# Optimization experiments

Measured on AMD Instinct MI355X. Metric: run time of the kernel, lower is better.

Reference implementation:

```python
import jax, jax.numpy as jnp
import numpy as np

B, H, W = 8, 64, 64
DIM, NH, WS = 768, 12, 14
HD = DIM // NH            # head dim = 64
N = WS * WS               # tokens per window = 196
PAD = (WS - H % WS) % WS  # 6 -> padded grid 70
HP, WP = H + PAD, W + PAD
NW = (HP // WS) * (WP // WS)  # 25 windows
EPS = 1e-5


def _layer_norm(x, w, b):
    mu = x.mean(-1, keepdims=True)
    var = ((x - mu) ** 2).mean(-1, keepdims=True)
    return (x - mu) * jax.lax.rsqrt(var + EPS) * w + b


def _window_partition(x):
    # [B,H,W,C] -> [B*NW, WS, WS, C] with zero padding
    x = jnp.pad(x, ((0, 0), (0, PAD), (0, PAD), (0, 0)))
    x = x.reshape(B, HP // WS, WS, WP // WS, WS, DIM)
    return x.transpose(0, 1, 3, 2, 4, 5).reshape(-1, WS, WS, DIM)


def _window_unpartition(w):
    x = w.reshape(B, HP // WS, WP // WS, WS, WS, DIM)
    x = x.transpose(0, 1, 3, 2, 4, 5).reshape(B, HP, WP, DIM)
    return x[:, :H, :W, :]


def _rel_table(rel_pos):
    # get_rel_pos with q_size==k_size==WS, rel_pos already (2*WS-1, HD):
    # Rh[i,j] = rel_pos[i - j + WS - 1]; summed over channel dim (batched_index_and_sum sums last dim)
    coords = jnp.arange(WS)[:, None] - jnp.arange(WS)[None, :] + (WS - 1)
    return rel_pos[coords].sum(-1)  # (WS, WS)


def _attention(w, q_idx, k_idx, qkv_w, qkv_b, proj_w, proj_b, rel_h, rel_w):
    Bp = w.shape[0]  # B*NW
    xq = w.reshape(Bp, N, DIM)
    qkv = xq @ qkv_w + qkv_b                                  # (Bp, N, 3*DIM)
    qkv = qkv.reshape(Bp, N, 3, NH, HD).transpose(2, 0, 3, 1, 4)
    qkv = qkv.reshape(3, Bp * NH, N, HD)
    q, k, v = qkv[0], qkv[1], qkv[2]
    scale = HD ** -0.5
    attn = jnp.einsum('bqc,bkc->bqk', q * scale, k)           # (Bp*NH, N, N)
    # decomposed rel-pos bias via irregular per-batch index gather
    Sh, Sw = _rel_table(rel_h), _rel_table(rel_w)
    qr, qc = q_idx // WS, q_idx % WS                          # (Bp*NH, N)
    kr, kc = k_idx // WS, k_idx % WS
    bias = Sh[qr[:, :, None], kr[:, None, :]] + Sw[qc[:, :, None], kc[:, None, :]]
    attn = jax.nn.softmax(attn + bias, axis=-1)
    out = jnp.einsum('bqk,bkc->bqc', attn, v)                 # (Bp*NH, N, HD)
    out = out.reshape(Bp, NH, N, HD).transpose(0, 2, 1, 3).reshape(Bp, WS, WS, DIM)
    return out @ proj_w + proj_b


def _block(x, q_idx, k_idx, ln1_w, ln1_b, ln2_w, ln2_b, qkv_w, qkv_b,
           proj_w, proj_b, rel_h, rel_w, mlp_w1, mlp_b1, mlp_w2, mlp_b2):
    shortcut = x
    h = _layer_norm(x, ln1_w, ln1_b)
    win = _window_partition(h)
    win = _attention(win, q_idx, k_idx, qkv_w, qkv_b, proj_w, proj_b, rel_h, rel_w)
    h = _window_unpartition(win)
    x = shortcut + h
    m = _layer_norm(x, ln2_w, ln2_b)
    m = jax.nn.gelu(m @ mlp_w1 + mlp_b1, approximate=False) @ mlp_w2 + mlp_b2
    return x + m


def setup_inputs() -> dict:
    key = jax.random.key(0)
    ks = jax.random.split(key, 12)
    f = lambda k, s: jax.random.normal(k, s, jnp.float32) * 0.02
    return {
        'x': jax.random.normal(ks[0], (B, H, W, DIM), jnp.float32),
        'q_idx': jnp.sort(jax.random.randint(ks[1], (B * NW * NH, N), 0, N), axis=-1),
        'k_idx': jnp.sort(jax.random.randint(ks[2], (B * NW * NH, N), 0, N), axis=-1),
        'ln1_w': jnp.ones((DIM,), jnp.float32), 'ln1_b': jnp.zeros((DIM,), jnp.float32),
        'ln2_w': jnp.ones((DIM,), jnp.float32), 'ln2_b': jnp.zeros((DIM,), jnp.float32),
        'qkv_w': f(ks[3], (DIM, 3 * DIM)), 'qkv_b': jnp.zeros((3 * DIM,), jnp.float32),
        'proj_w': f(ks[4], (DIM, DIM)), 'proj_b': jnp.zeros((DIM,), jnp.float32),
        'rel_h': f(ks[5], (2 * WS - 1, HD)), 'rel_w': f(ks[6], (2 * WS - 1, HD)),
        'mlp_w1': f(ks[7], (DIM, 4 * DIM)), 'mlp_b1': jnp.zeros((4 * DIM,), jnp.float32),
        'mlp_w2': f(ks[8], (4 * DIM, DIM)), 'mlp_b2': jnp.zeros((DIM,), jnp.float32),
    }


def reference(x, q_idx, k_idx, ln1_w, ln1_b, ln2_w, ln2_b, qkv_w, qkv_b,
              proj_w, proj_b, rel_h, rel_w, mlp_w1, mlp_b1, mlp_w2, mlp_b2):
    return _block(x, q_idx, k_idx, ln1_w, ln1_b, ln2_w, ln2_b, qkv_w, qkv_b,
                  proj_w, proj_b, rel_h, rel_w, mlp_w1, mlp_b1, mlp_w2, mlp_b2)
```

## Files before the change

kernel.cpp:

```cpp
#include <hip/hip_runtime.h>


typedef __bf16 bf16x8 __attribute__((ext_vector_type(8)));
typedef float f32x4 __attribute__((ext_vector_type(4)));
typedef unsigned int u32x4 __attribute__((ext_vector_type(4)));

__device__ __forceinline__ unsigned short f2bf(float f) {
  unsigned int u = __builtin_bit_cast(unsigned int, f);
  u += 0x7FFFu + ((u >> 16) & 1u);
  return (unsigned short)(u >> 16);
}

__device__ __forceinline__ bf16x8 ld8(const unsigned short* p) {
  return __builtin_bit_cast(bf16x8, *(const u32x4*)p);
}

__global__ void transpose_w(const float* __restrict__ in,
                            unsigned short* __restrict__ out, int K, int N) {
  __shared__ float t[32][33];
  int n = blockIdx.x * 32 + threadIdx.x;
  int kb = blockIdx.y * 32;
#pragma unroll
  for (int i = 0; i < 4; i++) {
    int k = kb + threadIdx.y + i * 8;
    t[threadIdx.y + i * 8][threadIdx.x] = in[(size_t)k * N + n];
  }
  __syncthreads();
  int k2 = kb + threadIdx.x;
#pragma unroll
  for (int i = 0; i < 4; i++) {
    int n2 = blockIdx.x * 32 + threadIdx.y + i * 8;
    out[(size_t)n2 * K + k2] = f2bf(t[threadIdx.x][threadIdx.y + i * 8]);
  }
}

__global__ void shsw_kernel(const float* __restrict__ rh,
                            const float* __restrict__ rw,
                            float* __restrict__ o) {
  int t = threadIdx.x;
  if (t < 196) {
    int i = t / 14, j = t % 14, d = i - j + 13;
    float sh = 0.f, sw = 0.f;
    for (int c = 0; c < 64; c++) {
      sh += rh[d * 64 + c];
      sw += rw[d * 64 + c];
    }
    o[t] = sh;
    o[196 + t] = sw;
  }
}

__global__ __launch_bounds__(256) void ln_kernel(
    const float* __restrict__ xin, const float* __restrict__ w,
    const float* __restrict__ b, unsigned short* __restrict__ out,
    int windowed) {
  __shared__ float red[8];
  __shared__ float ms[2];
  const int tid = threadIdx.x;
  const int blk = blockIdx.x;
  const float* xr = xin + (size_t)blk * 768;
  float v0 = xr[tid], v1 = xr[tid + 256], v2 = xr[tid + 512];
  float s = v0 + v1 + v2;
  float q = v0 * v0 + v1 * v1 + v2 * v2;
#pragma unroll
  for (int off = 32; off > 0; off >>= 1) {
    s += __shfl_down(s, off, 64);
    q += __shfl_down(q, off, 64);
  }
  const int wv = tid >> 6, lane = tid & 63;
  if (lane == 0) { red[wv] = s; red[4 + wv] = q; }
  __syncthreads();
  if (tid == 0) {
    float st = red[0] + red[1] + red[2] + red[3];
    float qt = red[4] + red[5] + red[6] + red[7];
    float mu = st * (1.0f / 768.0f);
    float var = qt * (1.0f / 768.0f) - mu * mu;
    ms[0] = mu;
    ms[1] = rsqrtf(var + 1e-5f);
  }
  __syncthreads();
  float mu = ms[0], sc = ms[1];
  unsigned short* dst;
  if (windowed) {
    int bb = blk >> 12, rem = blk & 4095, h = rem >> 6, ww = rem & 63;
    int win = (bb * 5 + h / 14) * 5 + ww / 14;
    int t = (h % 14) * 14 + (ww % 14);
    dst = out + ((size_t)win * 196 + t) * 768;
  } else {
    dst = out + (size_t)blk * 768;
  }
  dst[tid] = f2bf((v0 - mu) * sc * w[tid] + b[tid]);
  dst[tid + 256] = f2bf((v1 - mu) * sc * w[tid + 256] + b[tid + 256]);
  dst[tid + 512] = f2bf((v2 - mu) * sc * w[tid + 512] + b[tid + 512]);
}

template <int EPI>
__global__ __launch_bounds__(256, 2) void gemm_bt(
    const unsigned short* __restrict__ A, const unsigned short* __restrict__ Bt,
    const float* __restrict__ bias, int M, int N, int K,
    unsigned short* __restrict__ obf, float* __restrict__ of,
    const float* __restrict__ resid) {
  __shared__ __align__(16) unsigned short As[128 * 40];
  __shared__ __align__(16) unsigned short Bs[128 * 40];
  const int tid = threadIdx.x;
  const int lane = tid & 63, wv = tid >> 6;
  const int ln15 = lane & 15, quad = lane >> 4;
  const int wm = wv & 1, wn = wv >> 1;
  const int m0 = blockIdx.y * 128, n0 = blockIdx.x * 128;

  const int ra0 = tid >> 2, ka0 = (tid & 3) * 8;
  const int ra1 = ra0 + 64;
  const unsigned short* pA0 = A + (size_t)min(m0 + ra0, M - 1) * K + ka0;
  const unsigned short* pA1 = A + (size_t)min(m0 + ra1, M - 1) * K + ka0;
  const unsigned short* pB0 = Bt + (size_t)(n0 + ra0) * K + ka0;
  const unsigned short* pB1 = Bt + (size_t)(n0 + ra1) * K + ka0;

  const f32x4 fz = {0.f, 0.f, 0.f, 0.f};
  f32x4 acc[4][4];
#pragma unroll
  for (int i = 0; i < 4; i++)
#pragma unroll
    for (int j = 0; j < 4; j++) acc[i][j] = fz;

  u32x4 va0 = *(const u32x4*)(pA0);
  u32x4 va1 = *(const u32x4*)(pA1);
  u32x4 vb0 = *(const u32x4*)(pB0);
  u32x4 vb1 = *(const u32x4*)(pB1);

  for (int kt = 0; kt < K; kt += 32) {
    __syncthreads();
    *(u32x4*)(As + ra0 * 40 + ka0) = va0;
    *(u32x4*)(As + ra1 * 40 + ka0) = va1;
    *(u32x4*)(Bs + ra0 * 40 + ka0) = vb0;
    *(u32x4*)(Bs + ra1 * 40 + ka0) = vb1;
    __syncthreads();
    if (kt + 32 < K) {
      va0 = *(const u32x4*)(pA0 + kt + 32);
      va1 = *(const u32x4*)(pA1 + kt + 32);
      vb0 = *(const u32x4*)(pB0 + kt + 32);
      vb1 = *(const u32x4*)(pB1 + kt + 32);
    }
    bf16x8 af[4], bv[4];
#pragma unroll
    for (int t = 0; t < 4; t++) {
      af[t] = ld8(As + (wm * 64 + t * 16 + ln15) * 40 + quad * 8);
      bv[t] = ld8(Bs + (wn * 64 + t * 16 + ln15) * 40 + quad * 8);
    }
#pragma unroll
    for (int i = 0; i < 4; i++)
#pragma unroll
      for (int j = 0; j < 4; j++)
        acc[i][j] =
            __builtin_amdgcn_mfma_f32_16x16x32_bf16(af[i], bv[j], acc[i][j], 0, 0, 0);
  }

#pragma unroll
  for (int i = 0; i < 4; i++) {
#pragma unroll
    for (int j = 0; j < 4; j++) {
      const int col = n0 + wn * 64 + j * 16 + ln15;
      const float bc = bias[col];
#pragma unroll
      for (int g = 0; g < 4; g++) {
        const int row = m0 + wm * 64 + i * 16 + quad * 4 + g;
        if (row >= M) continue;
        float v = acc[i][j][g] + bc;
        if constexpr (EPI == 0) {
          obf[(size_t)row * N + col] = f2bf(v);
        } else if constexpr (EPI == 2) {
          float gl = 0.5f * v * (1.0f + erff(v * 0.70710678118f));
          obf[(size_t)row * N + col] = f2bf(gl);
        } else if constexpr (EPI == 1) {
          int win = row / 196, t = row - win * 196;
          int b = win / 25, wg = win - b * 25;
          int wr = wg / 5, wc = wg - wr * 5;
          int h = wr * 14 + t / 14;
          int w = wc * 14 + (t % 14);
          if (h < 64 && w < 64) {
            size_t oi = (((size_t)(b * 64 + h)) * 64 + w) * 768 + col;
            of[oi] = v + resid[oi];
          }
        } else {
          size_t oi = (size_t)row * N + col;
          of[oi] += v;
        }
      }
    }
  }
}

__global__ __launch_bounds__(256, 2) void attn_kernel(
    const unsigned short* __restrict__ qkv, const int* __restrict__ q_idx,
    const int* __restrict__ k_idx, const float* __restrict__ shsw,
    unsigned short* __restrict__ attnout) {
  __shared__ __align__(16) unsigned short Vt[64][232];
  __shared__ __align__(16) unsigned short Pst[4][16 * 232];
  __shared__ float Shs[196], Sws[196];
  __shared__ short qr14a[208], qc14a[208], kra[208], kca[208];

  const int tid = threadIdx.x;
  const int blk = blockIdx.x;
  const int win = blk / 12, head = blk % 12;
  const int lane = tid & 63, wv = tid >> 6;
  const int ln15 = lane & 15, quad = lane >> 4;
  const unsigned short* qg = qkv + (size_t)win * 196 * 2304;

  {
    unsigned int* vz = (unsigned int*)&Vt[0][0];
    for (int i = tid; i < 64 * 232 / 2; i += 256) vz[i] = 0u;
    unsigned int* pz = (unsigned int*)&Pst[0][0];
    for (int i = tid; i < 4 * 16 * 232 / 2; i += 256) pz[i] = 0u;
  }
  for (int i = tid; i < 196 * 64; i += 256) {
    int r = i >> 6, c = i & 63;
    Vt[c][r] = qg[(size_t)r * 2304 + 1536 + head * 64 + c];
  }
  for (int i = tid; i < 208; i += 256) {
    if (i < 196) {
      Shs[i] = shsw[i];
      Sws[i] = shsw[196 + i];
    }
    int q = (i < 196) ? q_idx[(size_t)blk * 196 + i] : 0;
    int k = (i < 196) ? k_idx[(size_t)blk * 196 + i] : 0;
    qr14a[i] = (short)((q / 14) * 14);
    qc14a[i] = (short)((q % 14) * 14);
    kra[i] = (short)(k / 14);
    kca[i] = (short)(k % 14);
  }
  __syncthreads();

  const f32x4 fz = {0.f, 0.f, 0.f, 0.f};
  unsigned short* strip = &Pst[wv][0];

  for (int mt = wv; mt < 13; mt += 4) {
    int qrow = mt * 16 + ln15;
    int qrc = (qrow < 196) ? qrow : 0;
    const unsigned short* qrp = qg + (size_t)qrc * 2304 + head * 64 + quad * 8;
    bf16x8 aq0 = ld8(qrp);
    bf16x8 aq1 = ld8(qrp + 32);

    f32x4 sacc[13];
#pragma unroll
    for (int nt = 0; nt < 13; nt++) {
      sacc[nt] = fz;
      int krow = nt * 16 + ln15;
      if (krow > 195) krow = 0;
      const unsigned short* krp =
          qg + (size_t)krow * 2304 + 768 + head * 64 + quad * 8;
      bf16x8 bk0 = ld8(krp);
      bf16x8 bk1 = ld8(krp + 32);
      sacc[nt] = __builtin_amdgcn_mfma_f32_16x16x32_bf16(aq0, bk0, sacc[nt], 0, 0, 0);
      sacc[nt] = __builtin_amdgcn_mfma_f32_16x16x32_bf16(aq1, bk1, sacc[nt], 0, 0, 0);
    }

    const int r0 = mt * 16 + quad * 4;
    int qi[4], qci[4];
#pragma unroll
    for (int g = 0; g < 4; g++) {
      qi[g] = qr14a[r0 + g];
      qci[g] = qc14a[r0 + g];
    }
    float rmax[4] = {-1e30f, -1e30f, -1e30f, -1e30f};
#pragma unroll
    for (int nt = 0; nt < 13; nt++) {
      int col = nt * 16 + ln15;
      int kr_ = kra[col], kc_ = kca[col];
#pragma unroll
      for (int g = 0; g < 4; g++) {
        float v = sacc[nt][g] * 0.125f + Shs[qi[g] + kr_] + Sws[qci[g] + kc_];
        if (col >= 196) v = -1e30f;
        sacc[nt][g] = v;
        rmax[g] = fmaxf(rmax[g], v);
      }
    }
#pragma unroll
    for (int off = 1; off < 16; off <<= 1)
#pragma unroll
      for (int g = 0; g < 4; g++)
        rmax[g] = fmaxf(rmax[g], __shfl_xor(rmax[g], off, 16));
    float rsum[4] = {0.f, 0.f, 0.f, 0.f};
#pragma unroll
    for (int nt = 0; nt < 13; nt++) {
      int col = nt * 16 + ln15;
#pragma unroll
      for (int g = 0; g < 4; g++) {
        float p = (col >= 196) ? 0.f : __expf(sacc[nt][g] - rmax[g]);
        sacc[nt][g] = p;
        rsum[g] += p;
      }
    }
#pragma unroll
    for (int off = 1; off < 16; off <<= 1)
#pragma unroll
      for (int g = 0; g < 4; g++) rsum[g] += __shfl_xor(rsum[g], off, 16);
    float rinv[4];
#pragma unroll
    for (int g = 0; g < 4; g++) rinv[g] = 1.0f / rsum[g];

#pragma unroll
    for (int nt = 0; nt < 13; nt++) {
      int col = nt * 16 + ln15;
#pragma unroll
      for (int g = 0; g < 4; g++)
        strip[(quad * 4 + g) * 232 + col] = f2bf(sacc[nt][g] * rinv[g]);
    }

    f32x4 oacc[4];
#pragma unroll
    for (int c4 = 0; c4 < 4; c4++) oacc[c4] = fz;
#pragma unroll
    for (int ks = 0; ks < 7; ks++) {
      bf16x8 ap = ld8(strip + ln15 * 232 + ks * 32 + quad * 8);
#pragma unroll
      for (int c4 = 0; c4 < 4; c4++) {
        bf16x8 bvv = ld8(&Vt[c4 * 16 + ln15][ks * 32 + quad * 8]);
        oacc[c4] = __builtin_amdgcn_mfma_f32_16x16x32_bf16(ap, bvv, oacc[c4], 0, 0, 0);
      }
    }
#pragma unroll
    for (int c4 = 0; c4 < 4; c4++)
#pragma unroll
      for (int g = 0; g < 4; g++) {
        int row = r0 + g;
        if (row < 196)
          attnout[((size_t)win * 196 + row) * 768 + head * 64 + c4 * 16 + ln15] =
              f2bf(oacc[c4][g]);
      }
  }
}

extern "C" void kernel_launch(void* const* d_in, const int* in_sizes, int n_in,
                              void* d_out, int out_size, void* d_ws,
                              size_t ws_size, hipStream_t stream) {
  const float* x = (const float*)d_in[0];
  const int* q_idx = (const int*)d_in[1];
  const int* k_idx = (const int*)d_in[2];
  const float* ln1w = (const float*)d_in[3];
  const float* ln1b = (const float*)d_in[4];
  const float* ln2w = (const float*)d_in[5];
  const float* ln2b = (const float*)d_in[6];
  const float* qkvw = (const float*)d_in[7];
  const float* qkvb = (const float*)d_in[8];
  const float* projw = (const float*)d_in[9];
  const float* projb = (const float*)d_in[10];
  const float* relh = (const float*)d_in[11];
  const float* relw = (const float*)d_in[12];
  const float* w1 = (const float*)d_in[13];
  const float* b1 = (const float*)d_in[14];
  const float* w2 = (const float*)d_in[15];
  const float* b2 = (const float*)d_in[16];
  float* out = (float*)d_out;

  char* ws = (char*)d_ws;
  unsigned short* xw = (unsigned short*)ws;
  const size_t offA = 60211200;
  unsigned short* qkv = (unsigned short*)(ws + offA);
  const size_t offB = offA + 201326592;
  unsigned short* qkvwt = (unsigned short*)(ws + offB);
  unsigned short* projwt = qkvwt + 2304 * 768;
  unsigned short* w1t = projwt + 768 * 768;
  unsigned short* w2t = w1t + 3072 * 768;
  float* shsw = (float*)(w2t + 768 * 3072);

  unsigned short* attnout = xw;
  unsigned short* ln2buf = xw;
  unsigned short* mlp1 = qkv;

  hipMemsetAsync(xw, 0, (size_t)39200 * 768 * 2, stream);

  dim3 tb(32, 8);
  transpose_w<<<dim3(2304 / 32, 768 / 32), tb, 0, stream>>>(qkvw, qkvwt, 768, 2304);
  transpose_w<<<dim3(768 / 32, 768 / 32), tb, 0, stream>>>(projw, projwt, 768, 768);
  transpose_w<<<dim3(3072 / 32, 768 / 32), tb, 0, stream>>>(w1, w1t, 768, 3072);
  transpose_w<<<dim3(768 / 32, 3072 / 32), tb, 0, stream>>>(w2, w2t, 3072, 768);
  shsw_kernel<<<1, 256, 0, stream>>>(relh, relw, shsw);

  ln_kernel<<<32768, 256, 0, stream>>>(x, ln1w, ln1b, xw, 1);

  gemm_bt<0><<<dim3(18, 307), 256, 0, stream>>>(xw, qkvwt, qkvb, 39200, 2304,
                                                768, qkv, nullptr, nullptr);
  attn_kernel<<<2400, 256, 0, stream>>>(qkv, q_idx, k_idx, shsw, attnout);

  gemm_bt<1><<<dim3(6, 307), 256, 0, stream>>>(attnout, projwt, projb, 39200,
                                               768, 768, nullptr, out, x);
  ln_kernel<<<32768, 256, 0, stream>>>(out, ln2w, ln2b, ln2buf, 0);

  gemm_bt<2><<<dim3(24, 256), 256, 0, stream>>>(ln2buf, w1t, b1, 32768, 3072,
                                                768, mlp1, nullptr, nullptr);
  gemm_bt<3><<<dim3(6, 256), 256, 0, stream>>>(mlp1, w2t, b2, 32768, 768, 3072,
                                               nullptr, out, nullptr);
  (void)in_sizes; (void)n_in; (void)out_size; (void)ws_size;
}
```

Before: 1.289 ms.

## Load GEMM tiles directly into LDS and remap blocks across XCDs

The GEMM main loop now uses global_load_lds (direct global-to-LDS DMA) instead of register-staged loads, and drops the row padding of 40 in favour of a dense 32-element row stride. It also remaps block IDs so that consecutive tiles land on the same XCD, to improve L2 locality. The register prefetch of the next K tile is removed, so global load latency is no longer overlapped with compute within a block. The unpadded LDS layout may cause bank conflicts on the MFMA fragment reads. There is also no explicit vmcnt wait before the barrier that follows the async LDS writes, which risks reading stale tile data.

Result: no change. 1.267 ms (-1.7%).

```diff
diff --git a/kernel.cpp b/kernel.cpp
--- a/kernel.cpp
+++ b/kernel.cpp
@@ -13,6 +13,13 @@
 
 __device__ __forceinline__ bf16x8 ld8(const unsigned short* p) {
   return __builtin_bit_cast(bf16x8, *(const u32x4*)p);
+}
+
+__device__ __forceinline__ void gload_lds16(const unsigned short* g,
+                                            unsigned short* l) {
+  __builtin_amdgcn_global_load_lds(
+      (const __attribute__((address_space(1))) unsigned int*)g,
+      (__attribute__((address_space(3))) unsigned int*)l, 16, 0, 0);
 }
 
 __global__ void transpose_w(const float* __restrict__ in,
@@ -100,20 +107,31 @@
     const float* __restrict__ bias, int M, int N, int K,
     unsigned short* __restrict__ obf, float* __restrict__ of,
     const float* __restrict__ resid) {
-  __shared__ __align__(16) unsigned short As[128 * 40];
-  __shared__ __align__(16) unsigned short Bs[128 * 40];
+  __shared__ __align__(16) unsigned short As[128 * 32];
+  __shared__ __align__(16) unsigned short Bs[128 * 32];
   const int tid = threadIdx.x;
   const int lane = tid & 63, wv = tid >> 6;
   const int ln15 = lane & 15, quad = lane >> 4;
   const int wm = wv & 1, wn = wv >> 1;
-  const int m0 = blockIdx.y * 128, n0 = blockIdx.x * 128;
+
+  int bid = blockIdx.y * gridDim.x + blockIdx.x;
+  {
+    const int nwg = gridDim.x * gridDim.y;
+    const int q = nwg >> 3, r = nwg & 7;
+    const int xcd = bid & 7, lo = bid >> 3;
+    bid = (xcd < r ? xcd * (q + 1) : r * (q + 1) + (xcd - r) * q) + lo;
+  }
+  const int m0 = (bid / gridDim.x) * 128, n0 = (bid % gridDim.x) * 128;
 
   const int ra0 = tid >> 2, ka0 = (tid & 3) * 8;
-  const int ra1 = ra0 + 64;
   const unsigned short* pA0 = A + (size_t)min(m0 + ra0, M - 1) * K + ka0;
-  const unsigned short* pA1 = A + (size_t)min(m0 + ra1, M - 1) * K + ka0;
+  const unsigned short* pA1 = A + (size_t)min(m0 + ra0 + 64, M - 1) * K + ka0;
   const unsigned short* pB0 = Bt + (size_t)(n0 + ra0) * K + ka0;
-  const unsigned short* pB1 = Bt + (size_t)(n0 + ra1) * K + ka0;
+  const unsigned short* pB1 = Bt + (size_t)(n0 + ra0 + 64) * K + ka0;
+  unsigned short* lA0 = As + tid * 8;
+  unsigned short* lA1 = As + 2048 + tid * 8;
+  unsigned short* lB0 = Bs + tid * 8;
+  unsigned short* lB1 = Bs + 2048 + tid * 8;
 
   const f32x4 fz = {0.f, 0.f, 0.f, 0.f};
   f32x4 acc[4][4];
@@ -122,29 +140,18 @@
 #pragma unroll
     for (int j = 0; j < 4; j++) acc[i][j] = fz;
 
-  u32x4 va0 = *(const u32x4*)(pA0);
-  u32x4 va1 = *(const u32x4*)(pA1);
-  u32x4 vb0 = *(const u32x4*)(pB0);
-  u32x4 vb1 = *(const u32x4*)(pB1);
-
   for (int kt = 0; kt < K; kt += 32) {
     __syncthreads();
-    *(u32x4*)(As + ra0 * 40 + ka0) = va0;
-    *(u32x4*)(As + ra1 * 40 + ka0) = va1;
-    *(u32x4*)(Bs + ra0 * 40 + ka0) = vb0;
-    *(u32x4*)(Bs + ra1 * 40 + ka0) = vb1;
+    gload_lds16(pA0 + kt, lA0);
+    gload_lds16(pA1 + kt, lA1);
+    gload_lds16(pB0 + kt, lB0);
+    gload_lds16(pB1 + kt, lB1);
     __syncthreads();
-    if (kt + 32 < K) {
-      va0 = *(const u32x4*)(pA0 + kt + 32);
-      va1 = *(const u32x4*)(pA1 + kt + 32);
-      vb0 = *(const u32x4*)(pB0 + kt + 32);
-      vb1 = *(const u32x4*)(pB1 + kt + 32);
-    }
     bf16x8 af[4], bv[4];
 #pragma unroll
     for (int t = 0; t < 4; t++) {
-      af[t] = ld8(As + (wm * 64 + t * 16 + ln15) * 40 + quad * 8);
-      bv[t] = ld8(Bs + (wn * 64 + t * 16 + ln15) * 40 + quad * 8);
+      af[t] = ld8(As + (wm * 64 + t * 16 + ln15) * 32 + quad * 8);
+      bv[t] = ld8(Bs + (wn * 64 + t * 16 + ln15) * 32 + quad * 8);
     }
 #pragma unroll
     for (int i = 0; i < 4; i++)
```
